# Kernel optimization log

Measured on AMD Instinct MI355X. Metric: run time of the kernel, lower is better.

Reference implementation:

```python
import jax, jax.numpy as jnp
import numpy as np

N, M, D = 1024, 32, 512
EPS = 1e-6


def setup_inputs() -> dict:
    key = jax.random.key(0)
    k1, = jax.random.split(key, 1)
    dvecs = jax.random.normal(k1, (N, M, D), dtype=jnp.float32)
    w = jnp.float32(10.0)
    b = jnp.float32(-5.0)
    return {"dvecs": dvecs, "w": w, "b": b}


def reference(dvecs, w, b):
    # dvecs: (N, M, D)
    n, m, d = dvecs.shape
    centroids = dvecs.mean(axis=1)                     # (N, D) full centroids
    # leave-one-out centroid for the reference utterance's own speaker
    c_loo = (dvecs.sum(axis=1, keepdims=True) - dvecs) / (m - 1)   # (N, M, D)

    e_norm = jnp.linalg.norm(dvecs, axis=-1)           # (N, M)
    c_norm = jnp.linalg.norm(centroids, axis=-1)       # (N,)
    c_loo_norm = jnp.linalg.norm(c_loo, axis=-1)       # (N, M)

    # cosine sim against all full centroids: (N, M, N)
    cos = jnp.einsum('jmd,kd->jmk', dvecs, centroids) / (
        e_norm[:, :, None] * c_norm[None, None, :])
    # replace the own-speaker entry with leave-one-out cosine
    loo_cos = jnp.einsum('jmd,jmd->jm', dvecs, c_loo) / (e_norm * c_loo_norm)
    jidx = jnp.arange(n)
    midx = jnp.arange(m)
    cos = cos.at[jidx[:, None], midx[None, :], jidx[:, None]].set(loo_cos)

    # torch.clamp(x, 1e-6) clamps the minimum only
    cos = jnp.maximum(cos, EPS) * w + b

    # softmax embed loss: L[j,i] = -log_softmax(cos[j,i,:])[j]
    logp = jax.nn.log_softmax(cos, axis=-1)
    L = -logp[jidx[:, None], midx[None, :], jidx[:, None]]
    return L.sum()
```

## Files before the change

kernel.cpp:

```cpp
#include <hip/hip_runtime.h>
#include <hip/hip_bf16.h>

#define NSPK 1024
#define MU 32
#define DIM 512
#define DIMP (DIM + 8)
#define NROW (NSPK * MU)
#define EPS 1e-6f

typedef __attribute__((ext_vector_type(4))) float f32x4;
typedef __attribute__((ext_vector_type(8))) short bf16x8;

#define GLOAD_LDS16(g, l)                                          \
  __builtin_amdgcn_global_load_lds(                                \
      (const __attribute__((address_space(1))) void*)(g),          \
      (__attribute__((address_space(3))) void*)(l), 16, 0, 0)

__device__ inline ushort f2bf(float x) {
  __hip_bfloat16 h = __float2bfloat16(x);
  return *reinterpret_cast<ushort*>(&h);
}

__global__ __launch_bounds__(256) void k_prep(
    const float* __restrict__ dvecs,
    ushort* __restrict__ Af,
    ushort* __restrict__ Bf,
    float* __restrict__ loo)
{
  const int j = blockIdx.x, t = threadIdx.x;
  __shared__ float sD[MU * DIMP];
  __shared__ float sS[DIM];
  __shared__ float sred[4];
  __shared__ float sS2v;
  __shared__ float sInv[MU];

  const float* base = dvecs + (size_t)j * (MU * DIM);

  float s0 = 0.f, s1 = 0.f;
  for (int m = 0; m < MU; ++m) {
    float a = base[m * DIM + t];
    float b = base[m * DIM + t + 256];
    sD[m * DIMP + t] = a;
    sD[m * DIMP + t + 256] = b;
    s0 += a; s1 += b;
  }
  sS[t] = s0; sS[t + 256] = s1;
  __syncthreads();

  float p = s0 * s0 + s1 * s1;
  for (int off = 32; off; off >>= 1) p += __shfl_down(p, off);
  if ((t & 63) == 0) sred[t >> 6] = p;
  __syncthreads();
  if (t == 0) sS2v = sred[0] + sred[1] + sred[2] + sred[3];
  __syncthreads();
  const float S2 = sS2v;

  const int g = t >> 3, l = t & 7;
  float dotS = 0.f, e2 = 0.f;
  for (int i = 0; i < DIM / 8; ++i) {
    int d = i * 8 + l;
    float ev = sD[g * DIMP + d];
    dotS += ev * sS[d];
    e2 += ev * ev;
  }
  for (int off = 4; off; off >>= 1) {
    dotS += __shfl_down(dotS, off);
    e2 += __shfl_down(e2, off);
  }
  if (l == 0) {
    float numer = dotS - e2;
    float d2 = fmaxf(S2 - 2.f * dotS + e2, 1e-30f);
    loo[j * MU + g] = numer / (sqrtf(e2) * sqrtf(d2));
    sInv[g] = 1.f / sqrtf(e2);
  }
  __syncthreads();

  for (int i = 0; i < 8; ++i) {
    int idx = i * 256 + t;
    int fragL = idx >> 6;
    int lane2 = idx & 63;
    int rbl = fragL >> 4, kf = fragL & 15;
    int m = rbl * 16 + (lane2 & 15);
    int k0 = kf * 32 + (lane2 >> 4) * 8;
    float inv = sInv[m];
    ushort tmp[8];
#pragma unroll
    for (int z = 0; z < 8; ++z) tmp[z] = f2bf(sD[m * DIMP + k0 + z] * inv);
    *(bf16x8*)&Af[(((size_t)(j * 2 + rbl) * 16 + kf) << 9) + lane2 * 8] =
        *(bf16x8*)tmp;
  }

  if (t < 64) {
    int kf = t >> 2, q = t & 3;
    int lane2 = q * 16 + (j & 15);
    float invc = 1.f / sqrtf(S2);
    int k0 = kf * 32 + q * 8;
    ushort tmp[8];
#pragma unroll
    for (int z = 0; z < 8; ++z) tmp[z] = f2bf(sS[k0 + z] * invc);
    *(bf16x8*)&Bf[(((size_t)(j >> 4) * 16 + kf) << 9) + lane2 * 8] =
        *(bf16x8*)tmp;
  }
}

__global__ __launch_bounds__(256, 1) void k_gemm(
    const ushort* __restrict__ Af,
    const ushort* __restrict__ Bf,
    const float* __restrict__ wp,
    float* __restrict__ part,
    float* __restrict__ diag)
{
  __shared__ ushort ldsA[3 * 8 * 512];
  __shared__ ushort ldsB[3 * 8 * 512];
  __shared__ float sPart[128][2];

  const int t = threadIdx.x;
  const int w = t >> 6, lane = t & 63;
  const int lr = lane & 15, lk = lane >> 4;
  const int wm = w >> 1, wn = w & 1;
  const int bid = blockIdx.x;
  const int xcd = bid & 7, ii = bid >> 3;
  const int rb = xcd * 32 + (ii >> 3);
  const int cb = ii & 7;

  f32x4 acc[4][4];
#pragma unroll
  for (int a = 0; a < 4; ++a)
#pragma unroll
    for (int b = 0; b < 4; ++b) acc[a][b] = (f32x4)0.f;

#define STAGE(kt, bi)                                                        \
  {                                                                          \
    _Pragma("unroll")                                                        \
    for (int r = 0; r < 2; ++r) {                                            \
      const int el = r * 4 + w;                                    \
      GLOAD_LDS16(                                                           \
          Af + (((size_t)(rb * 8 + el) * 16 + (kt)) << 9) + lane * 8,        \
          &ldsA[(bi) * 4096 + el * 512 + lane * 8]);                         \
      GLOAD_LDS16(                                                           \
          Bf + (((size_t)(cb * 8 + el) * 16 + (kt)) << 9) + lane * 8,        \
          &ldsB[(bi) * 4096 + el * 512 + lane * 8]);                         \
    }                                                                        \
  }

  STAGE(0, 0);
  STAGE(1, 1);

#pragma unroll
  for (int kt = 0; kt < 16; ++kt) {
    if (kt < 15) {
      asm volatile("s_waitcnt vmcnt(4)" ::: "memory");
    } else {
      asm volatile("s_waitcnt vmcnt(0)" ::: "memory");
    }
    __builtin_amdgcn_s_barrier();
    __builtin_amdgcn_sched_barrier(0);

    if (kt < 14) STAGE(kt + 2, (kt + 2) % 3);

    const ushort* lA = &ldsA[(kt % 3) * 4096];
    const ushort* lB = &ldsB[(kt % 3) * 4096];
    bf16x8 bfr[4];
#pragma unroll
    for (int nf = 0; nf < 4; ++nf)
      bfr[nf] = *(const bf16x8*)&lB[((wn * 4 + nf) << 9) + lane * 8];
#pragma unroll
    for (int mf = 0; mf < 4; ++mf) {
      const bf16x8 afr =
          *(const bf16x8*)&lA[((wm * 4 + mf) << 9) + lane * 8];
#pragma unroll
      for (int nf = 0; nf < 4; ++nf)
        acc[mf][nf] = __builtin_amdgcn_mfma_f32_16x16x32_bf16(
            afr, bfr[nf], acc[mf][nf], 0, 0, 0);
    }

    asm volatile("s_waitcnt lgkmcnt(0)" ::: "memory");
    __builtin_amdgcn_sched_barrier(0);
  }
#undef STAGE

  const float W = *wp;

  if (cb == (rb >> 5)) {
#pragma unroll
    for (int sp = 0; sp < 4; ++sp) {
      const int c = rb * 4 + sp;
      if (wm == (sp >> 1) && wn == ((c >> 6) & 1)) {
        const int nfo = (c >> 4) & 3;
#pragma unroll
        for (int mh = 0; mh < 2; ++mh) {
          f32x4 dsel = acc[(sp & 1) * 2 + mh][0];
#pragma unroll
          for (int nf = 1; nf < 4; ++nf)
            if (nf == nfo) dsel = acc[(sp & 1) * 2 + mh][nf];
          if (lr == (c & 15)) {
#pragma unroll
            for (int i = 0; i < 4; ++i)
              diag[c * 32 + mh * 16 + lk * 4 + i] = dsel[i];
          }
        }
      }
    }
  }

#pragma unroll
  for (int mf = 0; mf < 4; ++mf)
#pragma unroll
    for (int i = 0; i < 4; ++i) {
      float s = 0.f;
#pragma unroll
      for (int nf = 0; nf < 4; ++nf)
        s += __expf((fmaxf(acc[mf][nf][i], EPS) - 1.f) * W);
      s += __shfl_xor(s, 1);
      s += __shfl_xor(s, 2);
      s += __shfl_xor(s, 4);
      s += __shfl_xor(s, 8);
      if (lr == 0) sPart[wm * 64 + mf * 16 + lk * 4 + i][wn] = s;
    }
  __syncthreads();
  if (t < 128)
    part[(size_t)cb * NROW + rb * 128 + t] = sPart[t][0] + sPart[t][1];
}

__global__ __launch_bounds__(256) void k_final1(
    const float* __restrict__ part, const float* __restrict__ loo,
    const float* __restrict__ diag, const float* __restrict__ wp,
    float* __restrict__ p2)
{
  const int t = threadIdx.x;
  const int r = blockIdx.x * 256 + t;
  const float W = *wp;
  float s = 0.f;
#pragma unroll
  for (int c = 0; c < 8; ++c) s += part[(size_t)c * NROW + r];
  const float lt = (fmaxf(loo[r], EPS) - 1.f) * W;
  const float dt = (fmaxf(diag[r], EPS) - 1.f) * W;
  s += __expf(lt) - __expf(dt);
  float v = logf(s) - lt;
  __shared__ float red[4];
  for (int off = 32; off; off >>= 1) v += __shfl_down(v, off);
  if ((t & 63) == 0) red[t >> 6] = v;
  __syncthreads();
  if (t == 0) p2[blockIdx.x] = red[0] + red[1] + red[2] + red[3];
}

__global__ __launch_bounds__(128) void k_final2(
    const float* __restrict__ p2, float* __restrict__ out)
{
  const int t = threadIdx.x;
  float v = p2[t];
  for (int off = 32; off; off >>= 1) v += __shfl_down(v, off);
  __shared__ float red[2];
  if ((t & 63) == 0) red[t >> 6] = v;
  __syncthreads();
  if (t == 0) out[0] = red[0] + red[1];
}

extern "C" void kernel_launch(void* const* d_in, const int* in_sizes, int n_in,
                              void* d_out, int out_size, void* d_ws, size_t ws_size,
                              hipStream_t stream) {
  const float* dvecs = (const float*)d_in[0];
  const float* wptr  = (const float*)d_in[1];
  float* out = (float*)d_out;

  char* ws = (char*)d_ws;
  ushort* Af = (ushort*)ws;  ws += (size_t)NROW * DIM * sizeof(ushort);
  ushort* Bf = (ushort*)ws;  ws += (size_t)NSPK * DIM * sizeof(ushort);
  float* loo  = (float*)ws;  ws += (size_t)NROW * sizeof(float);
  float* diag = (float*)ws;  ws += (size_t)NROW * sizeof(float);
  float* part = (float*)ws;  ws += (size_t)8 * NROW * sizeof(float);
  float* p2   = (float*)ws;

  k_prep<<<NSPK, 256, 0, stream>>>(dvecs, Af, Bf, loo);
  k_gemm<<<2048, 256, 0, stream>>>(Af, Bf, wptr, part, diag);
  k_final1<<<NROW / 256, 256, 0, stream>>>(part, loo, diag, wptr, p2);
  k_final2<<<1, 128, 0, stream>>>(p2, out);
}
```

Baseline: 70.04 us.

## Double-buffer MFMA operand registers and deepen LDS prefetch in GEMM loop

```diff
diff --git a/kernel.cpp b/kernel.cpp
--- a/kernel.cpp
+++ b/kernel.cpp
@@ -129,26 +129,50 @@
 #pragma unroll
     for (int b = 0; b < 4; ++b) acc[a][b] = (f32x4)0.f;
 
-#define STAGE(kt, bi)                                                        \
-  {                                                                          \
-    _Pragma("unroll")                                                        \
-    for (int r = 0; r < 2; ++r) {                                            \
-      const int el = r * 4 + w;                                    \
-      GLOAD_LDS16(                                                           \
-          Af + (((size_t)(rb * 8 + el) * 16 + (kt)) << 9) + lane * 8,        \
-          &ldsA[(bi) * 4096 + el * 512 + lane * 8]);                         \
-      GLOAD_LDS16(                                                           \
-          Bf + (((size_t)(cb * 8 + el) * 16 + (kt)) << 9) + lane * 8,        \
-          &ldsB[(bi) * 4096 + el * 512 + lane * 8]);                         \
-    }                                                                        \
+  const ushort* gA0 = Af + (((size_t)(rb * 8 + w) * 16) << 9) + lane * 8;
+  const ushort* gA1 = Af + (((size_t)(rb * 8 + w + 4) * 16) << 9) + lane * 8;
+  const ushort* gB0 = Bf + (((size_t)(cb * 8 + w) * 16) << 9) + lane * 8;
+  const ushort* gB1 = Bf + (((size_t)(cb * 8 + w + 4) * 16) << 9) + lane * 8;
+  ushort* dA0 = &ldsA[w * 512 + lane * 8];
+  ushort* dA1 = &ldsA[(w + 4) * 512 + lane * 8];
+  ushort* dB0 = &ldsB[w * 512 + lane * 8];
+  ushort* dB1 = &ldsB[(w + 4) * 512 + lane * 8];
+
+#define STAGE(kt, bi)                                   \
+  {                                                     \
+    GLOAD_LDS16(gA0 + (kt) * 512, dA0 + (bi) * 4096);   \
+    GLOAD_LDS16(gA1 + (kt) * 512, dA1 + (bi) * 4096);   \
+    GLOAD_LDS16(gB0 + (kt) * 512, dB0 + (bi) * 4096);   \
+    GLOAD_LDS16(gB1 + (kt) * 512, dB1 + (bi) * 4096);   \
+  }
+
+  bf16x8 afr[2][4], bfr[2][4];
+  const ushort* lA0 = &ldsA[(wm * 4) * 512 + lane * 8];
+  const ushort* lB0 = &ldsB[(wn * 4) * 512 + lane * 8];
+
+#define DSREAD(set, bi)                                                   \
+  {                                                                       \
+    _Pragma("unroll")                                                     \
+    for (int nf = 0; nf < 4; ++nf)                                        \
+      bfr[set][nf] = *(const bf16x8*)(lB0 + (bi) * 4096 + nf * 512);      \
+    _Pragma("unroll")                                                     \
+    for (int mf = 0; mf < 4; ++mf)                                        \
+      afr[set][mf] = *(const bf16x8*)(lA0 + (bi) * 4096 + mf * 512);      \
   }
 
   STAGE(0, 0);
   STAGE(1, 1);
+  asm volatile("s_waitcnt vmcnt(4)" ::: "memory");
+  __builtin_amdgcn_s_barrier();
+  __builtin_amdgcn_sched_barrier(0);
+  STAGE(2, 2);
+  DSREAD(0, 0);
+  asm volatile("s_waitcnt lgkmcnt(0)" ::: "memory");
+  __builtin_amdgcn_sched_barrier(0);
 
 #pragma unroll
   for (int kt = 0; kt < 16; ++kt) {
-    if (kt < 15) {
+    if (kt < 14) {
       asm volatile("s_waitcnt vmcnt(4)" ::: "memory");
     } else {
       asm volatile("s_waitcnt vmcnt(0)" ::: "memory");
@@ -156,28 +180,25 @@
     __builtin_amdgcn_s_barrier();
     __builtin_amdgcn_sched_barrier(0);
 
-    if (kt < 14) STAGE(kt + 2, (kt + 2) % 3);
-
-    const ushort* lA = &ldsA[(kt % 3) * 4096];
-    const ushort* lB = &ldsB[(kt % 3) * 4096];
-    bf16x8 bfr[4];
-#pragma unroll
-    for (int nf = 0; nf < 4; ++nf)
-      bfr[nf] = *(const bf16x8*)&lB[((wn * 4 + nf) << 9) + lane * 8];
-#pragma unroll
-    for (int mf = 0; mf < 4; ++mf) {
-      const bf16x8 afr =
-          *(const bf16x8*)&lA[((wm * 4 + mf) << 9) + lane * 8];
+    if (kt <= 12) STAGE(kt + 3, (kt + 3) % 3);
+    if (kt < 15) DSREAD((kt + 1) & 1, (kt + 1) % 3);
+
+    __builtin_amdgcn_s_setprio(1);
+#pragma unroll
+    for (int mf = 0; mf < 4; ++mf)
 #pragma unroll
       for (int nf = 0; nf < 4; ++nf)
         acc[mf][nf] = __builtin_amdgcn_mfma_f32_16x16x32_bf16(
-            afr, bfr[nf], acc[mf][nf], 0, 0, 0);
-    }
-
-    asm volatile("s_waitcnt lgkmcnt(0)" ::: "memory");
-    __builtin_amdgcn_sched_barrier(0);
+            afr[kt & 1][mf], bfr[kt & 1][nf], acc[mf][nf], 0, 0, 0);
+    __builtin_amdgcn_s_setprio(0);
+
+    if (kt < 15) {
+      asm volatile("s_waitcnt lgkmcnt(0)" ::: "memory");
+      __builtin_amdgcn_sched_barrier(0);
+    }
   }
 #undef STAGE
+#undef DSREAD
 
   const float W = *wp;
 
```

Result: no change. 69.09 us (-1.4%).
